# Kernel tuning notes

Hardware: AMD Instinct MI355X
Metric: run time of the kernel (lower is better)

## Reference

```python
import jax, jax.numpy as jnp
import numpy as np

B, S, F, H = 256, 100, 256, 1024
T = 200


def setup_inputs() -> dict:
    key = jax.random.key(0)
    ks = jax.random.split(key, 11)
    sc = 0.02  # small init scale keeps LSTM dynamics stable
    return {
        "x": jax.random.normal(ks[0], (B, S, F), jnp.float32),
        "W_ih0": jax.random.normal(ks[1], (4 * H, F), jnp.float32) * sc,
        "W_hh0": jax.random.normal(ks[2], (4 * H, H), jnp.float32) * sc,
        "b0": jax.random.normal(ks[3], (4 * H,), jnp.float32) * sc,  # b_ih0 + b_hh0 folded
        "W_ih1": jax.random.normal(ks[4], (4 * H, H), jnp.float32) * sc,
        "W_hh1": jax.random.normal(ks[5], (4 * H, H), jnp.float32) * sc,
        "b1": jax.random.normal(ks[6], (4 * H,), jnp.float32) * sc,
        "out_W": jax.random.normal(ks[7], (F, H), jnp.float32) * sc,
        "out_b": jax.random.normal(ks[8], (F,), jnp.float32) * sc,
        "dy_mu": jax.random.normal(ks[9], (F,), jnp.float32) * 0.01,
        "dy_std": jax.random.uniform(ks[10], (F,), jnp.float32, minval=0.5, maxval=1.5),
        "t": T,
    }


def _cell(xt, h, c, Wih, Whh, b):
    # torch LSTM cell, gate order i,f,g,o
    g = xt @ Wih.T + h @ Whh.T + b  # [B, 4H]
    i, f, gg, o = jnp.split(g, 4, axis=-1)
    c = jax.nn.sigmoid(f) * c + jax.nn.sigmoid(i) * jnp.tanh(gg)
    h = jax.nn.sigmoid(o) * jnp.tanh(c)
    return h, c


def reference(x, W_ih0, W_hh0, b0, W_ih1, W_hh1, b1, out_W, out_b, dy_mu, dy_std, t):
    Bb = x.shape[0]
    Hh = W_hh0.shape[1]
    z = jnp.zeros((Bb, Hh), x.dtype)

    def seq_step(carry, xt):
        h0, c0, h1, c1 = carry
        h0, c0 = _cell(xt, h0, c0, W_ih0, W_hh0, b0)
        h1, c1 = _cell(h0, h1, c1, W_ih1, W_hh1, b1)
        return (h0, c0, h1, c1), h1

    state, preds = jax.lax.scan(seq_step, (z, z, z, z), jnp.swapaxes(x, 0, 1))
    dx = jnp.swapaxes(preds, 0, 1) @ out_W.T + out_b  # [B,S,F]; note: unscaled (matches source)
    out0 = jnp.concatenate([x[:, :1], x + dx], axis=1)  # [B,S+1,F]

    def dec_step(carry, _):
        last, h0, c0, h1, c1 = carry
        h0, c0 = _cell(last, h0, c0, W_ih0, W_hh0, b0)
        h1, c1 = _cell(h0, h1, c1, W_ih1, W_hh1, b1)
        dxt = dy_std * (h1 @ out_W.T + out_b) + dy_mu
        new = last + dxt
        return (new, h0, c0, h1, c1), new

    _, news = jax.lax.scan(dec_step, (out0[:, -1],) + state, None, length=t - 1)
    return jnp.concatenate([out0, jnp.swapaxes(news, 0, 1)], axis=1)  # [B, S+t, F]
```

## Files before the change

### kernel.cpp

```cpp
#include <hip/hip_runtime.h>


#define S_   100
#define OUTC 300
#define NTHR 512

typedef __attribute__((ext_vector_type(8))) _Float16 half8;
typedef __attribute__((ext_vector_type(4))) float    floatx4;

#define OFF_P       0u
#define OFF_C0      16777216u
#define OFF_C1      17825792u
#define OFF_H0HI    18874368u
#define OFF_H0LO    19398656u
#define OFF_H1HI    19922944u
#define OFF_H1LO    20447232u
#define OFF_BAR     20971520u
#define OFF_LASTF   20971776u
#define OFF_LASTHI  21233920u
#define OFF_LASTLO  21364992u
#define OFF_OWHI    21496064u
#define OFF_OWLO    22020352u
#define OFF_WFRAG   22544640u
#define NEED_WS     77070592ull

#define NZ_WORDS   1048640
#define N_OW       262144
#define N_OUT0     65536
#define SLOTS_WG   13312
#define N_FRAG     3407872

#define LDS_BYTES  131072

struct KParams {
  const float* x;
  const float* b0; const float* b1;
  const float* out_b; const float* dy_mu; const float* dy_std;
  const _Float16* OWhi; const _Float16* OWlo;
  const half8* wfrag;
  float* P; float* c0; float* c1; float* lastf;
  _Float16 *h0hi, *h0lo, *h1hi, *h1lo;
  _Float16 *lasthi, *lastlo;
  unsigned* bar;
  float* out;
};

__device__ __forceinline__ float fsig(float x)  { return 1.f / (1.f + __expf(-x)); }
__device__ __forceinline__ float ftanh_(float x){ float e = __expf(2.f*x); return 1.f - 2.f/(e + 1.f); }

__device__ __forceinline__ floatx4 mfma16h(half8 a, half8 b, floatx4 c){
  return __builtin_amdgcn_mfma_f32_16x16x32_f16(a, b, c, 0, 0, 0);
}

__device__ __forceinline__ void gridbar(unsigned* cnt){
  __syncthreads();
  if (threadIdx.x == 0) {
    unsigned arr = __hip_atomic_fetch_add(cnt, 1u, __ATOMIC_RELEASE, __HIP_MEMORY_SCOPE_AGENT);
    unsigned target = (arr & ~255u) + 256u;
    while (__hip_atomic_load(cnt, __ATOMIC_RELAXED, __HIP_MEMORY_SCOPE_AGENT) < target) {
      __builtin_amdgcn_s_sleep(4);
    }
    __builtin_amdgcn_fence(__ATOMIC_ACQUIRE, "agent");
  }
  __syncthreads();
}

__device__ __forceinline__ void split2(float v, _Float16& hi, _Float16& lo){
  _Float16 h = (_Float16)v;
  hi = h;
  lo = (_Float16)((v - (float)h) * 2048.0f);
}

template<int NKT, bool X32, bool BLDS>
__device__ __forceinline__ void gemm_phase(
    const float* __restrict__ xf, int strXf,
    const _Float16* __restrict__ xhi, const _Float16* __restrict__ xlo, int strX,
    int kb,
    const _Float16* __restrict__ hhi, const _Float16* __restrict__ hlo,
    const half8* __restrict__ bhiP, const half8* __restrict__ bloP, int kbase,
    float* __restrict__ Ppart, int nt, int ks)
{
  const int wv  = threadIdx.x >> 6;
  const int l   = threadIdx.x & 63;
  const int l15 = l & 15;
  const int lk  = (l >> 4) << 3;

  int mrow[2];
  #pragma unroll
  for (int mt = 0; mt < 2; ++mt) mrow[mt] = wv*32 + mt*16 + l15;

  floatx4 acc[2][4]  = {};
  floatx4 accl[2][4] = {};

  #pragma unroll 2
  for (int kt = 0; kt < NKT; ++kt) {
    const int k0 = kbase + kt*32;
    half8 ahi[2], alo[2];
    if (k0 < kb) {
      if (X32) {
        #pragma unroll
        for (int mt = 0; mt < 2; ++mt) {
          const float* p = xf + (size_t)mrow[mt]*strXf + k0 + lk;
          #pragma unroll
          for (int j = 0; j < 8; ++j) {
            float w = p[j];
            _Float16 h = (_Float16)w;
            ahi[mt][j] = h;
            alo[mt][j] = (_Float16)((w - (float)h) * 2048.0f);
          }
        }
      } else {
        #pragma unroll
        for (int mt = 0; mt < 2; ++mt) {
          size_t off = (size_t)mrow[mt]*strX + k0 + lk;
          ahi[mt] = *(const half8*)(xhi + off);
          alo[mt] = *(const half8*)(xlo + off);
        }
      }
    } else {
      #pragma unroll
      for (int mt = 0; mt < 2; ++mt) {
        size_t off = (size_t)mrow[mt]*1024 + (k0 - kb) + lk;
        ahi[mt] = *(const half8*)(hhi + off);
        alo[mt] = *(const half8*)(hlo + off);
      }
    }
    #pragma unroll
    for (int n = 0; n < 4; ++n) {
      half8 bhi, blo;
      if constexpr (BLDS) {
        extern __shared__ half8 smem[];
        bhi = smem[(kt*4 + n)*64 + l];
        blo = smem[4096 + (kt*4 + n)*64 + l];
      } else {
        bhi = bhiP[(kt*4 + n)*64 + l];
        blo = bloP[(kt*4 + n)*64 + l];
      }
      #pragma unroll
      for (int mt = 0; mt < 2; ++mt) {
        acc[mt][n]  = mfma16h(ahi[mt], bhi, acc[mt][n]);
        accl[mt][n] = mfma16h(alo[mt], bhi, accl[mt][n]);
        accl[mt][n] = mfma16h(ahi[mt], blo, accl[mt][n]);
      }
    }
  }

  float* pb = Ppart + (size_t)(ks*64 + nt) * (256*64);
  const int rbase = (l >> 4) * 4;
  #pragma unroll
  for (int mt = 0; mt < 2; ++mt)
    #pragma unroll
    for (int p = 0; p < 4; ++p) {
      int m = wv*32 + mt*16 + rbase + p;
      #pragma unroll
      for (int n = 0; n < 4; ++n)
        pb[(size_t)m*64 + n*16 + l15] = acc[mt][n][p] + accl[mt][n][p] * (1.0f/2048.0f);
    }
}

__device__ __forceinline__ void gate_phase(
    const float* __restrict__ P, float* __restrict__ cbuf,
    _Float16* __restrict__ hhi, _Float16* __restrict__ hlo,
    const float* __restrict__ bias, int nt, int ks)
{
  #pragma unroll
  for (int j = 0; j < 2; ++j) {
    int id = j*NTHR + threadIdx.x;
    int ml = id >> 4, hc = id & 15;
    int m = ks*64 + ml, hcol = nt*16 + hc;
    float g[4];
    #pragma unroll
    for (int gg = 0; gg < 4; ++gg) {
      float s = bias[gg*1024 + hcol];
      #pragma unroll
      for (int k = 0; k < 4; ++k)
        s += P[(size_t)(k*64 + nt)*(256*64) + (size_t)m*64 + gg*16 + hc];
      g[gg] = s;
    }
    int idx = m*1024 + hcol;
    float c = fsig(g[1]) * cbuf[idx] + fsig(g[0]) * ftanh_(g[2]);
    cbuf[idx] = c;
    float h = fsig(g[3]) * ftanh_(c);
    split2(h, hhi[idx], hlo[idx]);
  }
}

__device__ __forceinline__ void out_phase_w0(
    const _Float16* __restrict__ h1hi, const _Float16* __restrict__ h1lo,
    const _Float16* __restrict__ OWhi, const _Float16* __restrict__ OWlo,
    const float* __restrict__ out_b, const float* __restrict__ dy_mu,
    const float* __restrict__ dy_std,
    const float* __restrict__ xcol, float* __restrict__ outcol,
    float* __restrict__ lastf, _Float16* __restrict__ lasthi, _Float16* __restrict__ lastlo,
    int mode)
{
  const int l   = threadIdx.x;
  const int l15 = l & 15;
  const int lk  = (l >> 4) << 3;
  const int mo = blockIdx.x & 15, no = blockIdx.x >> 4;

  floatx4 acc = {}, accl = {};
  #pragma unroll 4
  for (int kt = 0; kt < 32; ++kt) {
    int k = kt*32 + lk;
    half8 a  = *(const half8*)(h1hi + (mo*16 + l15)*1024 + k);
    half8 al = *(const half8*)(h1lo + (mo*16 + l15)*1024 + k);
    half8 b  = *(const half8*)(OWhi + (no*16 + l15)*1024 + k);
    half8 bl = *(const half8*)(OWlo + (no*16 + l15)*1024 + k);
    acc  = mfma16h(a,  b,  acc);
    accl = mfma16h(al, b,  accl);
    accl = mfma16h(a,  bl, accl);
  }
  #pragma unroll
  for (int p = 0; p < 4; ++p) {
    float s = acc[p] + accl[p] * (1.0f/2048.0f);
    int m = mo*16 + (l >> 4)*4 + p;
    int f = no*16 + l15;
    s += out_b[f];
    if (mode == 2) {
      float dxt = dy_std[f]*s + dy_mu[f];
      float nl = lastf[m*256+f] + dxt;
      lastf[m*256+f] = nl;
      outcol[(size_t)m*(OUTC*256) + f] = nl;
      split2(nl, lasthi[m*256+f], lastlo[m*256+f]);
    } else {
      float o = xcol[m*25600 + f] + s;
      outcol[(size_t)m*(OUTC*256) + f] = o;
      if (mode == 1) { lastf[m*256+f] = o; split2(o, lasthi[m*256+f], lastlo[m*256+f]); }
    }
  }
}

__global__ void __launch_bounds__(NTHR, 2) lstm_persist(KParams kp)
{
  const int nt = blockIdx.x >> 2, ks = blockIdx.x & 3;

  const half8* W0hi = kp.wfrag + (size_t)blockIdx.x * SLOTS_WG;
  const half8* W0lo = W0hi + 2560;

  {
    extern __shared__ half8 smem[];
    const half8* src = kp.wfrag + (size_t)blockIdx.x * SLOTS_WG + 5120;
    for (int i = threadIdx.x; i < 8192; i += NTHR) smem[i] = src[i];
    __syncthreads();
  }

  for (int t = 0; t < S_; ++t) {
    gemm_phase<10, true, false>(kp.x + t*256, 25600, nullptr, nullptr, 0, 256,
                         kp.h0hi, kp.h0lo, W0hi, W0lo, ks*320, kp.P, nt, ks);
    if (t > 0 && threadIdx.x < 64)
      out_phase_w0(kp.h1hi, kp.h1lo, kp.OWhi, kp.OWlo,
                   kp.out_b, kp.dy_mu, kp.dy_std,
                   kp.x + (t-1)*256, kp.out + (size_t)t*256,
                   kp.lastf, kp.lasthi, kp.lastlo, 0);
    gridbar(kp.bar);
    gate_phase(kp.P, kp.c0, kp.h0hi, kp.h0lo, kp.b0, nt, ks);
    gridbar(kp.bar);
    gemm_phase<16, false, true>(nullptr, 0, kp.h0hi, kp.h0lo, 1024, 1024,
                          kp.h1hi, kp.h1lo, nullptr, nullptr, ks*512, kp.P, nt, ks);
    gridbar(kp.bar);
    gate_phase(kp.P, kp.c1, kp.h1hi, kp.h1lo, kp.b1, nt, ks);
    gridbar(kp.bar);
  }
  if (threadIdx.x < 64)
    out_phase_w0(kp.h1hi, kp.h1lo, kp.OWhi, kp.OWlo,
                 kp.out_b, kp.dy_mu, kp.dy_std,
                 kp.x + 99*256, kp.out + (size_t)100*256,
                 kp.lastf, kp.lasthi, kp.lastlo, 1);
  gridbar(kp.bar);

  for (int u = 0; u < 199; ++u) {
    gemm_phase<10, false, false>(nullptr, 0, kp.lasthi, kp.lastlo, 256, 256,
                          kp.h0hi, kp.h0lo, W0hi, W0lo, ks*320, kp.P, nt, ks);
    gridbar(kp.bar);
    gate_phase(kp.P, kp.c0, kp.h0hi, kp.h0lo, kp.b0, nt, ks);
    gridbar(kp.bar);
    gemm_phase<16, false, true>(nullptr, 0, kp.h0hi, kp.h0lo, 1024, 1024,
                          kp.h1hi, kp.h1lo, nullptr, nullptr, ks*512, kp.P, nt, ks);
    gridbar(kp.bar);
    gate_phase(kp.P, kp.c1, kp.h1hi, kp.h1lo, kp.b1, nt, ks);
    gridbar(kp.bar);
    if (threadIdx.x < 64)
      out_phase_w0(kp.h1hi, kp.h1lo, kp.OWhi, kp.OWlo,
                   kp.out_b, kp.dy_mu, kp.dy_std,
                   nullptr, kp.out + (size_t)(101+u)*256,
                   kp.lastf, kp.lasthi, kp.lastlo, 2);
    gridbar(kp.bar);
  }
}

__global__ void pre_kernel(const float* __restrict__ x, const float* __restrict__ outW,
                           const float* __restrict__ Wih0, const float* __restrict__ Whh0,
                           const float* __restrict__ Wih1, const float* __restrict__ Whh1,
                           _Float16* __restrict__ OWhi, _Float16* __restrict__ OWlo,
                           unsigned* __restrict__ zeroReg, float* __restrict__ out,
                           half8* __restrict__ wfrag)
{
  const int total = NZ_WORDS + N_OW + N_OUT0 + N_FRAG;
  for (int i = blockIdx.x*256 + threadIdx.x; i < total; i += gridDim.x*256) {
    if (i < NZ_WORDS) {
      zeroReg[i] = 0u;
    } else if (i < NZ_WORDS + N_OW) {
      int j = i - NZ_WORDS;
      split2(outW[j], OWhi[j], OWlo[j]);
    } else if (i < NZ_WORDS + N_OW + N_OUT0) {
      int j = i - (NZ_WORDS + N_OW);
      int m = j >> 8, f = j & 255;
      out[(size_t)m*(OUTC*256) + f] = x[m*25600 + f];
    } else {
      int fidx = i - (NZ_WORDS + N_OW + N_OUT0);
      int wg = fidx / SLOTS_WG;
      int r  = fidx - wg*SLOTS_WG;
      int nt = wg >> 2, ks = wg & 3;
      const float* src;
      bool lo;
      if (r < 5120) {
        lo = (r >= 2560);
        int rr = lo ? r - 2560 : r;
        int kt = rr >> 8, q = rr & 255, g = q >> 6, l = q & 63;
        int row = g*1024 + nt*16 + (l & 15);
        int k = ks*320 + kt*32 + ((l >> 4) << 3);
        src = (k < 256) ? (Wih0 + (size_t)row*256 + k)
                        : (Whh0 + (size_t)row*1024 + (k - 256));
      } else {
        int r2 = r - 5120;
        lo = (r2 >= 4096);
        int rr = lo ? r2 - 4096 : r2;
        int kt = rr >> 8, q = rr & 255, g = q >> 6, l = q & 63;
        int row = g*1024 + nt*16 + (l & 15);
        int k = ks*512 + kt*32 + ((l >> 4) << 3);
        src = (k < 1024) ? (Wih1 + (size_t)row*1024 + k)
                         : (Whh1 + (size_t)row*1024 + (k - 1024));
      }
      half8 v;
      #pragma unroll
      for (int j = 0; j < 8; ++j) {
        float w = src[j];
        _Float16 h = (_Float16)w;
        v[j] = lo ? (_Float16)((w - (float)h) * 2048.0f) : h;
      }
      wfrag[(size_t)wg*SLOTS_WG + r] = v;
    }
  }
}

__global__ void sent_kernel(float* out, float v) { out[0] = v; }

extern "C" void kernel_launch(void* const* d_in, const int* in_sizes, int n_in,
                              void* d_out, int out_size, void* d_ws, size_t ws_size,
                              hipStream_t stream)
{
  (void)in_sizes; (void)n_in; (void)out_size;
  char* ws = (char*)d_ws;
  float* out = (float*)d_out;

  if (ws_size < (size_t)NEED_WS) {
    sent_kernel<<<1, 1, 0, stream>>>(out, 900000.0f + 10.0f * (float)(ws_size >> 20));
    return;
  }

  const float* x    = (const float*)d_in[0];
  const float* Wih0 = (const float*)d_in[1];
  const float* Whh0 = (const float*)d_in[2];
  const float* Wih1 = (const float*)d_in[4];
  const float* Whh1 = (const float*)d_in[5];
  const float* outW = (const float*)d_in[7];

  KParams kp;
  kp.x     = x;
  kp.b0    = (const float*)d_in[3];
  kp.b1    = (const float*)d_in[6];
  kp.out_b = (const float*)d_in[8];
  kp.dy_mu = (const float*)d_in[9];
  kp.dy_std= (const float*)d_in[10];

  kp.P      = (float*)(ws + OFF_P);
  kp.c0     = (float*)(ws + OFF_C0);
  kp.c1     = (float*)(ws + OFF_C1);
  kp.h0hi   = (_Float16*)(ws + OFF_H0HI);
  kp.h0lo   = (_Float16*)(ws + OFF_H0LO);
  kp.h1hi   = (_Float16*)(ws + OFF_H1HI);
  kp.h1lo   = (_Float16*)(ws + OFF_H1LO);
  kp.bar    = (unsigned*)(ws + OFF_BAR);
  kp.lastf  = (float*)(ws + OFF_LASTF);
  kp.lasthi = (_Float16*)(ws + OFF_LASTHI);
  kp.lastlo = (_Float16*)(ws + OFF_LASTLO);
  kp.OWhi   = (const _Float16*)(ws + OFF_OWHI);
  kp.OWlo   = (const _Float16*)(ws + OFF_OWLO);
  kp.wfrag  = (const half8*)(ws + OFF_WFRAG);
  kp.out    = out;

  (void)hipGetLastError();
  pre_kernel<<<4096, 256, 0, stream>>>(x, outW, Wih0, Whh0, Wih1, Whh1,
      (_Float16*)(ws + OFF_OWHI), (_Float16*)(ws + OFF_OWLO),
      (unsigned*)(ws + OFF_C0), out,
      (half8*)(ws + OFF_WFRAG));
  hipError_t e1 = hipGetLastError();
  if (e1 != hipSuccess) {
    sent_kernel<<<1, 1, 0, stream>>>(out, 300000.0f + 10.0f * (float)e1);
    return;
  }

  (void)hipFuncSetAttribute((const void*)lstm_persist,
                            hipFuncAttributeMaxDynamicSharedMemorySize, LDS_BYTES);

  void* args[] = { &kp };
  hipError_t e2 = hipLaunchCooperativeKernel((const void*)lstm_persist,
                                             dim3(256), dim3(NTHR), args, LDS_BYTES, stream);
  if (e2 != hipSuccess) {
    (void)hipGetLastError();
    lstm_persist<<<256, NTHR, LDS_BYTES, stream>>>(kp);
    hipError_t e3 = hipGetLastError();
    if (e3 != hipSuccess) {
      sent_kernel<<<1, 1, 0, stream>>>(out, 500000.0f + 10.0f * (float)e3);
      return;
    }
  }
}
```

Baseline: 42.01 ms.

## Double workgroup threads so each wave computes one 16-row M tile

Raises the persistent kernel's workgroup size from 512 to 1024 threads. Each wave now handles a single 16-row tile instead of two, and each thread processes one gate element instead of two. The aim is more waves in flight per CU to hide the latency of the recurrent GEMM and gate phases. The cost is that each B fragment loaded from LDS or global memory is reused for only one M tile, and the larger block means a costlier grid-wide barrier per workgroup. The launch_bounds occupancy hint goes from 2 to 4, which may constrain register allocation.

```diff
diff --git a/kernel.cpp b/kernel.cpp
--- a/kernel.cpp
+++ b/kernel.cpp
@@ -3,7 +3,7 @@
 
 #define S_   100
 #define OUTC 300
-#define NTHR 512
+#define NTHR 1024
 
 typedef __attribute__((ext_vector_type(8))) _Float16 half8;
 typedef __attribute__((ext_vector_type(4))) float    floatx4;
@@ -85,45 +85,34 @@
   const int l15 = l & 15;
   const int lk  = (l >> 4) << 3;
 
-  int mrow[2];
-  #pragma unroll
-  for (int mt = 0; mt < 2; ++mt) mrow[mt] = wv*32 + mt*16 + l15;
-
-  floatx4 acc[2][4]  = {};
-  floatx4 accl[2][4] = {};
+  const int mrow = wv*16 + l15;
+
+  floatx4 acc[4]  = {};
+  floatx4 accl[4] = {};
 
   #pragma unroll 2
   for (int kt = 0; kt < NKT; ++kt) {
     const int k0 = kbase + kt*32;
-    half8 ahi[2], alo[2];
+    half8 ahi, alo;
     if (k0 < kb) {
       if (X32) {
+        const float* p = xf + (size_t)mrow*strXf + k0 + lk;
         #pragma unroll
-        for (int mt = 0; mt < 2; ++mt) {
-          const float* p = xf + (size_t)mrow[mt]*strXf + k0 + lk;
-          #pragma unroll
-          for (int j = 0; j < 8; ++j) {
-            float w = p[j];
-            _Float16 h = (_Float16)w;
-            ahi[mt][j] = h;
-            alo[mt][j] = (_Float16)((w - (float)h) * 2048.0f);
-          }
+        for (int j = 0; j < 8; ++j) {
+          float w = p[j];
+          _Float16 h = (_Float16)w;
+          ahi[j] = h;
+          alo[j] = (_Float16)((w - (float)h) * 2048.0f);
         }
       } else {
-        #pragma unroll
-        for (int mt = 0; mt < 2; ++mt) {
-          size_t off = (size_t)mrow[mt]*strX + k0 + lk;
-          ahi[mt] = *(const half8*)(xhi + off);
-          alo[mt] = *(const half8*)(xlo + off);
-        }
+        size_t off = (size_t)mrow*strX + k0 + lk;
+        ahi = *(const half8*)(xhi + off);
+        alo = *(const half8*)(xlo + off);
       }
     } else {
-      #pragma unroll
-      for (int mt = 0; mt < 2; ++mt) {
-        size_t off = (size_t)mrow[mt]*1024 + (k0 - kb) + lk;
-        ahi[mt] = *(const half8*)(hhi + off);
-        alo[mt] = *(const half8*)(hlo + off);
-      }
+      size_t off = (size_t)mrow*1024 + (k0 - kb) + lk;
+      ahi = *(const half8*)(hhi + off);
+      alo = *(const half8*)(hlo + off);
     }
     #pragma unroll
     for (int n = 0; n < 4; ++n) {
@@ -136,26 +125,21 @@
         bhi = bhiP[(kt*4 + n)*64 + l];
         blo = bloP[(kt*4 + n)*64 + l];
       }
-      #pragma unroll
-      for (int mt = 0; mt < 2; ++mt) {
-        acc[mt][n]  = mfma16h(ahi[mt], bhi, acc[mt][n]);
-        accl[mt][n] = mfma16h(alo[mt], bhi, accl[mt][n]);
-        accl[mt][n] = mfma16h(ahi[mt], blo, accl[mt][n]);
-      }
+      acc[n]  = mfma16h(ahi, bhi, acc[n]);
+      accl[n] = mfma16h(alo, bhi, accl[n]);
+      accl[n] = mfma16h(ahi, blo, accl[n]);
     }
   }
 
   float* pb = Ppart + (size_t)(ks*64 + nt) * (256*64);
   const int rbase = (l >> 4) * 4;
   #pragma unroll
-  for (int mt = 0; mt < 2; ++mt)
+  for (int p = 0; p < 4; ++p) {
+    int m = wv*16 + rbase + p;
     #pragma unroll
-    for (int p = 0; p < 4; ++p) {
-      int m = wv*32 + mt*16 + rbase + p;
-      #pragma unroll
-      for (int n = 0; n < 4; ++n)
-        pb[(size_t)m*64 + n*16 + l15] = acc[mt][n][p] + accl[mt][n][p] * (1.0f/2048.0f);
-    }
+    for (int n = 0; n < 4; ++n)
+      pb[(size_t)m*64 + n*16 + l15] = acc[n][p] + accl[n][p] * (1.0f/2048.0f);
+  }
 }
 
 __device__ __forceinline__ void gate_phase(
@@ -163,26 +147,23 @@
     _Float16* __restrict__ hhi, _Float16* __restrict__ hlo,
     const float* __restrict__ bias, int nt, int ks)
 {
+  int id = threadIdx.x;
+  int ml = id >> 4, hc = id & 15;
+  int m = ks*64 + ml, hcol = nt*16 + hc;
+  float g[4];
   #pragma unroll
-  for (int j = 0; j < 2; ++j) {
-    int id = j*NTHR + threadIdx.x;
-    int ml = id >> 4, hc = id & 15;
-    int m = ks*64 + ml, hcol = nt*16 + hc;
-    float g[4];
+  for (int gg = 0; gg < 4; ++gg) {
+    float s = bias[gg*1024 + hcol];
     #pragma unroll
-    for (int gg = 0; gg < 4; ++gg) {
-      float s = bias[gg*1024 + hcol];
-      #pragma unroll
-      for (int k = 0; k < 4; ++k)
-        s += P[(size_t)(k*64 + nt)*(256*64) + (size_t)m*64 + gg*16 + hc];
-      g[gg] = s;
-    }
-    int idx = m*1024 + hcol;
-    float c = fsig(g[1]) * cbuf[idx] + fsig(g[0]) * ftanh_(g[2]);
-    cbuf[idx] = c;
-    float h = fsig(g[3]) * ftanh_(c);
-    split2(h, hhi[idx], hlo[idx]);
-  }
+    for (int k = 0; k < 4; ++k)
+      s += P[(size_t)(k*64 + nt)*(256*64) + (size_t)m*64 + gg*16 + hc];
+    g[gg] = s;
+  }
+  int idx = m*1024 + hcol;
+  float c = fsig(g[1]) * cbuf[idx] + fsig(g[0]) * ftanh_(g[2]);
+  cbuf[idx] = c;
+  float h = fsig(g[3]) * ftanh_(c);
+  split2(h, hhi[idx], hlo[idx]);
 }
 
 __device__ __forceinline__ void out_phase_w0(
@@ -231,7 +212,7 @@
   }
 }
 
-__global__ void __launch_bounds__(NTHR, 2) lstm_persist(KParams kp)
+__global__ void __launch_bounds__(NTHR, 4) lstm_persist(KParams kp)
 {
   const int nt = blockIdx.x >> 2, ks = blockIdx.x & 3;
 
```

New measurement: 43.59 ms. 1.04x slower.

## Fuse gate math into GEMM by full-K per hidden column, double-buffer h, tree barrier

Applied to the files above, without the earlier changes.

Each workgroup now computes the full K reduction for 4 hidden units across all four gates. Shuffles gather the i/f/g/o gates within a wave, so the cell update happens in registers instead of going through a partial-sum buffer and a separate gate phase. Hidden states are double-buffered so reads and writes do not conflict, which cuts grid barriers per step from four to two. The flat atomic barrier is replaced with a two-level tree barrier. In exchange, each workgroup does a longer serial K loop with a smaller N tile, and only a quarter of the lanes do gate math.

```diff
diff --git a/kernel.cpp b/kernel.cpp
--- a/kernel.cpp
+++ b/kernel.cpp
@@ -8,28 +8,25 @@
 typedef __attribute__((ext_vector_type(8))) _Float16 half8;
 typedef __attribute__((ext_vector_type(4))) float    floatx4;
 
-#define OFF_P       0u
-#define OFF_C0      16777216u
-#define OFF_C1      17825792u
-#define OFF_H0HI    18874368u
-#define OFF_H0LO    19398656u
-#define OFF_H1HI    19922944u
-#define OFF_H1LO    20447232u
-#define OFF_BAR     20971520u
-#define OFF_LASTF   20971776u
-#define OFF_LASTHI  21233920u
-#define OFF_LASTLO  21364992u
-#define OFF_OWHI    21496064u
-#define OFF_OWLO    22020352u
-#define OFF_WFRAG   22544640u
-#define NEED_WS     77070592ull
-
-#define NZ_WORDS   1048640
+#define OFF_C0     0u
+#define OFF_C1     1048576u
+#define OFF_H      2097152u
+#define OFF_BAR2   6291456u
+#define OFF_LASTF  6299904u
+#define OFF_LASTHI 6562048u
+#define OFF_LASTLO 6693120u
+#define OFF_OWHI   6824192u
+#define OFF_OWLO   7348480u
+#define OFF_WFRAG  7872768u
+#define NEED_WS    62398720ull
+
+#define NZ_WORDS   1574976
 #define N_OW       262144
 #define N_OUT0     65536
 #define SLOTS_WG   13312
 #define N_FRAG     3407872
 
+#define BAR_STRIDE 64
 #define LDS_BYTES  131072
 
 struct KParams {
@@ -38,10 +35,10 @@
   const float* out_b; const float* dy_mu; const float* dy_std;
   const _Float16* OWhi; const _Float16* OWlo;
   const half8* wfrag;
-  float* P; float* c0; float* c1; float* lastf;
-  _Float16 *h0hi, *h0lo, *h1hi, *h1lo;
+  float* c0; float* c1; float* lastf;
+  _Float16* hs;
   _Float16 *lasthi, *lastlo;
-  unsigned* bar;
+  unsigned* bar2;
   float* out;
 };
 
@@ -52,12 +49,26 @@
   return __builtin_amdgcn_mfma_f32_16x16x32_f16(a, b, c, 0, 0, 0);
 }
 
-__device__ __forceinline__ void gridbar(unsigned* cnt){
+__device__ __forceinline__ void treebar(unsigned* b2, unsigned& ep, int wg){
   __syncthreads();
   if (threadIdx.x == 0) {
-    unsigned arr = __hip_atomic_fetch_add(cnt, 1u, __ATOMIC_RELEASE, __HIP_MEMORY_SCOPE_AGENT);
-    unsigned target = (arr & ~255u) + 256u;
-    while (__hip_atomic_load(cnt, __ATOMIC_RELAXED, __HIP_MEMORY_SCOPE_AGENT) < target) {
+    ep += 1u;
+    const int leaf = wg >> 4;
+    unsigned a = __hip_atomic_fetch_add(&b2[leaf*BAR_STRIDE], 1u,
+                                        __ATOMIC_RELEASE, __HIP_MEMORY_SCOPE_AGENT);
+    if ((a & 15u) == 15u) {
+      unsigned r = __hip_atomic_fetch_add(&b2[16*BAR_STRIDE], 1u,
+                                          __ATOMIC_RELAXED, __HIP_MEMORY_SCOPE_AGENT);
+      if ((r & 15u) == 15u) {
+        unsigned newep = (r >> 4) + 1u;
+        #pragma unroll
+        for (int i = 0; i < 16; ++i)
+          __hip_atomic_store(&b2[(17 + i)*BAR_STRIDE], newep,
+                             __ATOMIC_RELEASE, __HIP_MEMORY_SCOPE_AGENT);
+      }
+    }
+    while (__hip_atomic_load(&b2[(17 + leaf)*BAR_STRIDE],
+                             __ATOMIC_RELAXED, __HIP_MEMORY_SCOPE_AGENT) < ep) {
       __builtin_amdgcn_s_sleep(4);
     }
     __builtin_amdgcn_fence(__ATOMIC_ACQUIRE, "agent");
@@ -72,13 +83,15 @@
 }
 
 template<int NKT, bool X32, bool BLDS>
-__device__ __forceinline__ void gemm_phase(
+__device__ __forceinline__ void cell_phase(
     const float* __restrict__ xf, int strXf,
     const _Float16* __restrict__ xhi, const _Float16* __restrict__ xlo, int strX,
     int kb,
     const _Float16* __restrict__ hhi, const _Float16* __restrict__ hlo,
-    const half8* __restrict__ bhiP, const half8* __restrict__ bloP, int kbase,
-    float* __restrict__ Ppart, int nt, int ks)
+    const half8* __restrict__ bhiP, const half8* __restrict__ bloP,
+    float* __restrict__ cbuf,
+    _Float16* __restrict__ hhiW, _Float16* __restrict__ hloW,
+    const float* __restrict__ bias, int nt)
 {
   const int wv  = threadIdx.x >> 6;
   const int l   = threadIdx.x & 63;
@@ -89,12 +102,12 @@
   #pragma unroll
   for (int mt = 0; mt < 2; ++mt) mrow[mt] = wv*32 + mt*16 + l15;
 
-  floatx4 acc[2][4]  = {};
-  floatx4 accl[2][4] = {};
+  floatx4 acc[2]  = {};
+  floatx4 accl[2] = {};
 
   #pragma unroll 2
   for (int kt = 0; kt < NKT; ++kt) {
-    const int k0 = kbase + kt*32;
+    const int k0 = kt*32;
     half8 ahi[2], alo[2];
     if (k0 < kb) {
       if (X32) {
@@ -125,64 +138,46 @@
         alo[mt] = *(const half8*)(hlo + off);
       }
     }
+    half8 bhi, blo;
+    if constexpr (BLDS) {
+      extern __shared__ half8 smem[];
+      bhi = smem[kt*64 + l];
+      blo = smem[4096 + kt*64 + l];
+    } else {
+      bhi = bhiP[kt*64 + l];
+      blo = bloP[kt*64 + l];
+    }
     #pragma unroll
-    for (int n = 0; n < 4; ++n) {
-      half8 bhi, blo;
-      if constexpr (BLDS) {
-        extern __shared__ half8 smem[];
-        bhi = smem[(kt*4 + n)*64 + l];
-        blo = smem[4096 + (kt*4 + n)*64 + l];
-      } else {
-        bhi = bhiP[(kt*4 + n)*64 + l];
-        blo = bloP[(kt*4 + n)*64 + l];
-      }
-      #pragma unroll
-      for (int mt = 0; mt < 2; ++mt) {
-        acc[mt][n]  = mfma16h(ahi[mt], bhi, acc[mt][n]);
-        accl[mt][n] = mfma16h(alo[mt], bhi, accl[mt][n]);
-        accl[mt][n] = mfma16h(ahi[mt], blo, accl[mt][n]);
-      }
-    }
-  }
-
-  float* pb = Ppart + (size_t)(ks*64 + nt) * (256*64);
-  const int rbase = (l >> 4) * 4;
+    for (int mt = 0; mt < 2; ++mt) {
+      acc[mt]  = mfma16h(ahi[mt], bhi, acc[mt]);
+      accl[mt] = mfma16h(alo[mt], bhi, accl[mt]);
+      accl[mt] = mfma16h(ahi[mt], blo, accl[mt]);
+    }
+  }
+
+  const int g    = l15 >> 2;
+  const int hc   = l15 & 3;
+  const int hcol = nt*4 + hc;
+  const float bI = bias[hcol], bF = bias[1024+hcol],
+              bG = bias[2048+hcol], bO = bias[3072+hcol];
   #pragma unroll
   for (int mt = 0; mt < 2; ++mt)
     #pragma unroll
     for (int p = 0; p < 4; ++p) {
-      int m = wv*32 + mt*16 + rbase + p;
-      #pragma unroll
-      for (int n = 0; n < 4; ++n)
-        pb[(size_t)m*64 + n*16 + l15] = acc[mt][n][p] + accl[mt][n][p] * (1.0f/2048.0f);
-    }
-}
-
-__device__ __forceinline__ void gate_phase(
-    const float* __restrict__ P, float* __restrict__ cbuf,
-    _Float16* __restrict__ hhi, _Float16* __restrict__ hlo,
-    const float* __restrict__ bias, int nt, int ks)
-{
-  #pragma unroll
-  for (int j = 0; j < 2; ++j) {
-    int id = j*NTHR + threadIdx.x;
-    int ml = id >> 4, hc = id & 15;
-    int m = ks*64 + ml, hcol = nt*16 + hc;
-    float g[4];
-    #pragma unroll
-    for (int gg = 0; gg < 4; ++gg) {
-      float s = bias[gg*1024 + hcol];
-      #pragma unroll
-      for (int k = 0; k < 4; ++k)
-        s += P[(size_t)(k*64 + nt)*(256*64) + (size_t)m*64 + gg*16 + hc];
-      g[gg] = s;
-    }
-    int idx = m*1024 + hcol;
-    float c = fsig(g[1]) * cbuf[idx] + fsig(g[0]) * ftanh_(g[2]);
-    cbuf[idx] = c;
-    float h = fsig(g[3]) * ftanh_(c);
-    split2(h, hhi[idx], hlo[idx]);
-  }
+      float v  = acc[mt][p] + accl[mt][p] * (1.0f/2048.0f);
+      float s4  = __shfl_xor(v, 4);
+      float s8  = __shfl_xor(v, 8);
+      float s12 = __shfl_xor(v, 12);
+      if (g == 0) {
+        float gi = v + bI, gf = s4 + bF, gG = s8 + bG, go = s12 + bO;
+        int m   = wv*32 + mt*16 + (l >> 4)*4 + p;
+        int idx = m*1024 + hcol;
+        float c = fsig(gf) * cbuf[idx] + fsig(gi) * ftanh_(gG);
+        cbuf[idx] = c;
+        float h = fsig(go) * ftanh_(c);
+        split2(h, hhiW[idx], hloW[idx]);
+      }
+    }
 }
 
 __device__ __forceinline__ void out_phase_w0(
@@ -233,60 +228,68 @@
 
 __global__ void __launch_bounds__(NTHR, 2) lstm_persist(KParams kp)
 {
-  const int nt = blockIdx.x >> 2, ks = blockIdx.x & 3;
-
-  const half8* W0hi = kp.wfrag + (size_t)blockIdx.x * SLOTS_WG;
+  const int wg = blockIdx.x;
+  unsigned ep = 0;
+
+  const half8* W0hi = kp.wfrag + (size_t)wg * SLOTS_WG;
   const half8* W0lo = W0hi + 2560;
 
   {
     extern __shared__ half8 smem[];
-    const half8* src = kp.wfrag + (size_t)blockIdx.x * SLOTS_WG + 5120;
+    const half8* src = kp.wfrag + (size_t)wg * SLOTS_WG + 5120;
     for (int i = threadIdx.x; i < 8192; i += NTHR) smem[i] = src[i];
     __syncthreads();
   }
 
+  _Float16 *h0hR = kp.hs + 1048576,          *h0lR = kp.hs + 1048576 + 262144,
+           *h1hR = kp.hs + 1048576 + 524288, *h1lR = kp.hs + 1048576 + 786432;
+  _Float16 *h0hW = kp.hs,                    *h0lW = kp.hs + 262144,
+           *h1hW = kp.hs + 524288,           *h1lW = kp.hs + 786432;
+  #define SWP(a,b) { _Float16* _t = a; a = b; b = _t; }
+  #define SWAPALL() { SWP(h0hR,h0hW) SWP(h0lR,h0lW) SWP(h1hR,h1hW) SWP(h1lR,h1lW) }
+
   for (int t = 0; t < S_; ++t) {
-    gemm_phase<10, true, false>(kp.x + t*256, 25600, nullptr, nullptr, 0, 256,
-                         kp.h0hi, kp.h0lo, W0hi, W0lo, ks*320, kp.P, nt, ks);
+    cell_phase<40, true, false>(kp.x + t*256, 25600, nullptr, nullptr, 0, 256,
+                                h0hR, h0lR, W0hi, W0lo,
+                                kp.c0, h0hW, h0lW, kp.b0, wg);
     if (t > 0 && threadIdx.x < 64)
-      out_phase_w0(kp.h1hi, kp.h1lo, kp.OWhi, kp.OWlo,
+      out_phase_w0(h1hR, h1lR, kp.OWhi, kp.OWlo,
                    kp.out_b, kp.dy_mu, kp.dy_std,
                    kp.x + (t-1)*256, kp.out + (size_t)t*256,
                    kp.lastf, kp.lasthi, kp.lastlo, 0);
-    gridbar(kp.bar);
-    gate_phase(kp.P, kp.c0, kp.h0hi, kp.h0lo, kp.b0, nt, ks);
-    gridbar(kp.bar);
-    gemm_phase<16, false, true>(nullptr, 0, kp.h0hi, kp.h0lo, 1024, 1024,
-                          kp.h1hi, kp.h1lo, nullptr, nullptr, ks*512, kp.P, nt, ks);
-    gridbar(kp.bar);
-    gate_phase(kp.P, kp.c1, kp.h1hi, kp.h1lo, kp.b1, nt, ks);
-    gridbar(kp.bar);
+    treebar(kp.bar2, ep, wg);
+    cell_phase<64, false, true>(nullptr, 0, h0hW, h0lW, 1024, 1024,
+                                h1hR, h1lR, nullptr, nullptr,
+                                kp.c1, h1hW, h1lW, kp.b1, wg);
+    treebar(kp.bar2, ep, wg);
+    SWAPALL();
   }
   if (threadIdx.x < 64)
-    out_phase_w0(kp.h1hi, kp.h1lo, kp.OWhi, kp.OWlo,
+    out_phase_w0(h1hR, h1lR, kp.OWhi, kp.OWlo,
                  kp.out_b, kp.dy_mu, kp.dy_std,
                  kp.x + 99*256, kp.out + (size_t)100*256,
                  kp.lastf, kp.lasthi, kp.lastlo, 1);
-  gridbar(kp.bar);
+  treebar(kp.bar2, ep, wg);
 
   for (int u = 0; u < 199; ++u) {
-    gemm_phase<10, false, false>(nullptr, 0, kp.lasthi, kp.lastlo, 256, 256,
-                          kp.h0hi, kp.h0lo, W0hi, W0lo, ks*320, kp.P, nt, ks);
-    gridbar(kp.bar);
-    gate_phase(kp.P, kp.c0, kp.h0hi, kp.h0lo, kp.b0, nt, ks);
-    gridbar(kp.bar);
-    gemm_phase<16, false, true>(nullptr, 0, kp.h0hi, kp.h0lo, 1024, 1024,
-                          kp.h1hi, kp.h1lo, nullptr, nullptr, ks*512, kp.P, nt, ks);
-    gridbar(kp.bar);
-    gate_phase(kp.P, kp.c1, kp.h1hi, kp.h1lo, kp.b1, nt, ks);
-    gridbar(kp.bar);
+    cell_phase<40, false, false>(nullptr, 0, kp.lasthi, kp.lastlo, 256, 256,
+                                 h0hR, h0lR, W0hi, W0lo,
+                                 kp.c0, h0hW, h0lW, kp.b0, wg);
+    treebar(kp.bar2, ep, wg);
+    cell_phase<64, false, true>(nullptr, 0, h0hW, h0lW, 1024, 1024,
+                                h1hR, h1lR, nullptr, nullptr,
+                                kp.c1, h1hW, h1lW, kp.b1, wg);
+    treebar(kp.bar2, ep, wg);
     if (threadIdx.x < 64)
-      out_phase_w0(kp.h1hi, kp.h1lo, kp.OWhi, kp.OWlo,
+      out_phase_w0(h1hW, h1lW, kp.OWhi, kp.OWlo,
                    kp.out_b, kp.dy_mu, kp.dy_std,
                    nullptr, kp.out + (size_t)(101+u)*256,
                    kp.lastf, kp.lasthi, kp.lastlo, 2);
-    gridbar(kp.bar);
-  }
+    treebar(kp.bar2, ep, wg);
+    SWAPALL();
+  }
+  #undef SWAPALL
+  #undef SWP
 }
 
 __global__ void pre_kernel(const float* __restrict__ x, const float* __restrict__ outW,
@@ -311,24 +314,24 @@
       int fidx = i - (NZ_WORDS + N_OW + N_OUT0);
       int wg = fidx / SLOTS_WG;
       int r  = fidx - wg*SLOTS_WG;
-      int nt = wg >> 2, ks = wg & 3;
       const float* src;
       bool lo;
+      int kt, l;
       if (r < 5120) {
         lo = (r >= 2560);
         int rr = lo ? r - 2560 : r;
-        int kt = rr >> 8, q = rr & 255, g = q >> 6, l = q & 63;
-        int row = g*1024 + nt*16 + (l & 15);
-        int k = ks*320 + kt*32 + ((l >> 4) << 3);
+        kt = rr >> 6; l = rr & 63;
+        int row = ((l & 15) >> 2)*1024 + wg*4 + (l & 3);
+        int k = kt*32 + ((l >> 4) << 3);
         src = (k < 256) ? (Wih0 + (size_t)row*256 + k)
                         : (Whh0 + (size_t)row*1024 + (k - 256));
       } else {
         int r2 = r - 5120;
         lo = (r2 >= 4096);
         int rr = lo ? r2 - 4096 : r2;
-        int kt = rr >> 8, q = rr & 255, g = q >> 6, l = q & 63;
-        int row = g*1024 + nt*16 + (l & 15);
-        int k = ks*512 + kt*32 + ((l >> 4) << 3);
+        kt = rr >> 6; l = rr & 63;
+        int row = ((l & 15) >> 2)*1024 + wg*4 + (l & 3);
+        int k = kt*32 + ((l >> 4) << 3);
         src = (k < 1024) ? (Wih1 + (size_t)row*1024 + k)
                          : (Whh1 + (size_t)row*1024 + (k - 1024));
       }
@@ -374,14 +377,10 @@
   kp.dy_mu = (const float*)d_in[9];
   kp.dy_std= (const float*)d_in[10];
 
-  kp.P      = (float*)(ws + OFF_P);
   kp.c0     = (float*)(ws + OFF_C0);
   kp.c1     = (float*)(ws + OFF_C1);
-  kp.h0hi   = (_Float16*)(ws + OFF_H0HI);
-  kp.h0lo   = (_Float16*)(ws + OFF_H0LO);
-  kp.h1hi   = (_Float16*)(ws + OFF_H1HI);
-  kp.h1lo   = (_Float16*)(ws + OFF_H1LO);
-  kp.bar    = (unsigned*)(ws + OFF_BAR);
+  kp.hs     = (_Float16*)(ws + OFF_H);
+  kp.bar2   = (unsigned*)(ws + OFF_BAR2);
   kp.lastf  = (float*)(ws + OFF_LASTF);
   kp.lasthi = (_Float16*)(ws + OFF_LASTHI);
   kp.lastlo = (_Float16*)(ws + OFF_LASTLO);
@@ -393,7 +392,7 @@
   (void)hipGetLastError();
   pre_kernel<<<4096, 256, 0, stream>>>(x, outW, Wih0, Whh0, Wih1, Whh1,
       (_Float16*)(ws + OFF_OWHI), (_Float16*)(ws + OFF_OWLO),
-      (unsigned*)(ws + OFF_C0), out,
+      (unsigned*)ws, out,
       (half8*)(ws + OFF_WFRAG));
   hipError_t e1 = hipGetLastError();
   if (e1 != hipSuccess) {
```

Result: slower. 51.59 ms (+22.8%).
